# Performance work log

Measured on AMD Instinct MI355X. Metric: run time of the kernel, lower is better.

Reference implementation:

```python
import jax, jax.numpy as jnp
import numpy as np

SCALE = 0.125  # 1/sqrt(embed_dim=64), as passed to Self_Attn in the original


def setup_inputs() -> dict:
    key = jax.random.key(0)
    ks = jax.random.split(key, 6)
    B, S, N, D = 8192, 50, 100000, 64
    nodes = jax.random.randint(ks[0], (B,), 0, N)
    node_seq = jax.random.randint(ks[1], (B, S), 0, N)
    uv2e_weight = jax.random.normal(ks[2], (N, D), dtype=jnp.float32)
    feat_weight = jax.random.normal(ks[3], (N, D), dtype=jnp.float32)
    W1 = jax.random.normal(ks[4], (D, 2 * D), dtype=jnp.float32) * 0.05  # torch Linear weight (out, in)
    b1 = jax.random.normal(ks[5], (D,), dtype=jnp.float32) * 0.05
    return {"nodes": nodes, "node_seq": node_seq, "uv2e_weight": uv2e_weight,
            "feat_weight": feat_weight, "W1": W1, "b1": b1}


def reference(nodes, node_seq, uv2e_weight, feat_weight, W1, b1):
    # gather embeddings: q from self ids, k=v from padded/reversed neighbor sequences
    q = uv2e_weight[nodes]          # [B, D]
    k = uv2e_weight[node_seq]       # [B, S, D]
    v = k                           # same gather in the original
    # Self_Attn: scaled dot-product attention, query length 1 per node
    scores = jnp.einsum('bd,bsd->bs', q, k) * SCALE          # [B, S]
    attn = jax.nn.softmax(scores, axis=-1)                   # [B, S]
    folded = jnp.einsum('bs,bsd->bd', attn, v)                # [B, D]
    # self features (features(nodes).t() in torch yields [B, D])
    self_feats = feat_weight[nodes]                           # [B, D]
    combined = jnp.concatenate([self_feats, folded], axis=1)  # [B, 2D]
    out = jax.nn.relu(combined @ W1.T + b1)                   # [B, D]
    return out
```

## Files before the change

### kernel.cpp

```cpp
#include <hip/hip_runtime.h>
#include <hip/hip_fp16.h>
#include <math.h>


#define DD      64
#define SS      50
#define WPB     8
#define SCALE_L2E 0.180336880f

__device__ __forceinline__ float rdlane_f(float v, int l) {
    return __int_as_float(__builtin_amdgcn_readlane(__float_as_int(v), l));
}

template <int CTRL>
__device__ __forceinline__ float dpp_add(float x) {
    int r = __builtin_amdgcn_update_dpp(0, __float_as_int(x), CTRL, 0xf, 0xf, true);
    return x + __int_as_float(r);
}

__global__ __launch_bounds__(256) void cvt_f32_f16_kernel(
    const float* __restrict__ src, __half* __restrict__ dst, int n8)
{
    int i = blockIdx.x * blockDim.x + threadIdx.x;
    if (i >= n8) return;
    const float4* s4 = (const float4*)src;
    float4 a = s4[2 * i];
    float4 b = s4[2 * i + 1];
    union { __half h[8]; uint4 u; } o;
    o.h[0] = __float2half(a.x); o.h[1] = __float2half(a.y);
    o.h[2] = __float2half(a.z); o.h[3] = __float2half(a.w);
    o.h[4] = __float2half(b.x); o.h[5] = __float2half(b.y);
    o.h[6] = __float2half(b.z); o.h[7] = __float2half(b.w);
    *(uint4*)(dst + 8 * i) = o.u;
}

__global__ __launch_bounds__(512, 6) void folded_encoder_kernel(
    const int*    __restrict__ nodes,
    const int*    __restrict__ node_seq,
    const float*  __restrict__ uv2e,
    const float*  __restrict__ feat,
    const float*  __restrict__ W1,
    const float*  __restrict__ b1,
    const __half* __restrict__ ktab,
    float*        __restrict__ out,
    int B)
{
    __shared__ __align__(16) float Wsw[DD][2 * DD];
    __shared__ int seqbuf[WPB][SS + 2];

    const int tid = threadIdx.x;
    const int wid = tid >> 6;
    const int ln  = tid & 63;
    const int g   = ln >> 4;
    const int t   = ln & 15;

    const int row  = blockIdx.x * WPB + wid;
    const int rowc = row < B ? row : B - 1;

    #pragma unroll
    for (int rep = 0; rep < 16; ++rep) {
        int e = rep * 512 + tid;
        int o = e >> 7;
        int i = e & 127;
        int c = i >> 2, j = i & 3;
        Wsw[o][((c ^ (o & 7)) << 2) + j] = W1[e];
    }
    if (ln < SS) seqbuf[wid][ln] = node_seq[(size_t)rowc * SS + ln];

    const int nid = nodes[rowc];
    const float4 q4 = *(const float4*)(uv2e + (size_t)nid * DD + 4 * t);
    const float4 f4 = *(const float4*)(feat + (size_t)nid * DD + 4 * t);
    const float bias = b1[ln];

    __syncthreads();

    const int start = (25 * g) >> 1;
    const int len   = ((25 * (g + 1)) >> 1) - start;
    const int* sb   = &seqbuf[wid][0];

    int idxr[13];
    #pragma unroll
    for (int s = 0; s < 13; ++s)
        idxr[s] = sb[start + (s < len ? s : 0)];

    uint2 kr[13];
    #pragma unroll
    for (int s = 0; s < 13; ++s)
        kr[s] = *(const uint2*)(ktab + (size_t)idxr[s] * DD + 4 * t);

    float  l   = 0.f;
    float4 acc = make_float4(0.f, 0.f, 0.f, 0.f);
    #pragma unroll
    for (int s = 0; s < 13; ++s) {
        union { uint2 u; __half h[4]; } kw; kw.u = kr[s];
        float k0 = __half2float(kw.h[0]);
        float k1 = __half2float(kw.h[1]);
        float k2 = __half2float(kw.h[2]);
        float k3 = __half2float(kw.h[3]);

        float p = k0 * q4.x + k1 * q4.y + k2 * q4.z + k3 * q4.w;
        p = dpp_add<0xB1>(p);
        p = dpp_add<0x4E>(p);
        p = dpp_add<0x141>(p);
        p = dpp_add<0x140>(p);

        float e  = __builtin_amdgcn_exp2f(p * SCALE_L2E);
        float ee = (s < len) ? e : 0.f;
        l += ee;
        acc.x += ee * k0; acc.y += ee * k1;
        acc.z += ee * k2; acc.w += ee * k3;
    }

    l     += __shfl_xor(l, 16);     l     += __shfl_xor(l, 32);
    acc.x += __shfl_xor(acc.x, 16); acc.x += __shfl_xor(acc.x, 32);
    acc.y += __shfl_xor(acc.y, 16); acc.y += __shfl_xor(acc.y, 32);
    acc.z += __shfl_xor(acc.z, 16); acc.z += __shfl_xor(acc.z, 32);
    acc.w += __shfl_xor(acc.w, 16); acc.w += __shfl_xor(acc.w, 32);

    const float rl = 1.0f / l;
    const float4 fold = make_float4(acc.x * rl, acc.y * rl, acc.z * rl, acc.w * rl);

    float oa0 = bias, oa1 = 0.f;
    const float* wrow = &Wsw[ln][0];
    #pragma unroll
    for (int cc = 0; cc < 32; ++cc) {
        float4 w4 = *(const float4*)&wrow[((cc ^ (ln & 7)) << 2)];
        const int srcl = cc & 15;
        float c0, c1, c2, c3;
        if (cc < 16) {
            c0 = rdlane_f(f4.x, srcl); c1 = rdlane_f(f4.y, srcl);
            c2 = rdlane_f(f4.z, srcl); c3 = rdlane_f(f4.w, srcl);
        } else {
            c0 = rdlane_f(fold.x, srcl); c1 = rdlane_f(fold.y, srcl);
            c2 = rdlane_f(fold.z, srcl); c3 = rdlane_f(fold.w, srcl);
        }
        oa0 += c0 * w4.x + c1 * w4.y;
        oa1 += c2 * w4.z + c3 * w4.w;
    }

    if (row < B)
        out[(size_t)row * DD + ln] = fmaxf(oa0 + oa1, 0.f);
}

extern "C" void kernel_launch(void* const* d_in, const int* in_sizes, int n_in,
                              void* d_out, int out_size, void* d_ws, size_t ws_size,
                              hipStream_t stream) {
    const int*   nodes    = (const int*)  d_in[0];
    const int*   node_seq = (const int*)  d_in[1];
    const float* uv2e     = (const float*)d_in[2];
    const float* feat     = (const float*)d_in[3];
    const float* W1       = (const float*)d_in[4];
    const float* b1       = (const float*)d_in[5];
    float*       out      = (float*)d_out;
    __half*      ktab     = (__half*)d_ws;

    const int B  = in_sizes[0];
    const int NE = in_sizes[2];
    const int n8 = NE / 8;

    cvt_f32_f16_kernel<<<(n8 + 255) / 256, 256, 0, stream>>>(uv2e, ktab, n8);

    const int blocks = (B + WPB - 1) / WPB;
    folded_encoder_kernel<<<blocks, 512, 0, stream>>>(
        nodes, node_seq, uv2e, feat, W1, b1, ktab, out, B);
}
```

Before: 108.3 us.

## Pre-gather query/self features in prep kernel and process two row batches per block

The conversion kernel becomes a combined prep kernel that also gathers the uv2e and feat rows for each node into a contiguous qf buffer. The main kernel now handles two batches of 8 rows per block, which spreads the shared-memory W1 load (now float4-vectorised) across more work. It also reads node_seq indices directly from global memory instead of staging them in shared memory. The block count assumes B is divisible by 16 and the row<B guard no longer protects the q/f loads; the extra qf round-trip adds memory traffic.

```diff
diff --git a/kernel.cpp b/kernel.cpp
--- a/kernel.cpp
+++ b/kernel.cpp
@@ -6,6 +6,7 @@
 #define DD      64
 #define SS      50
 #define WPB     8
+#define BATCHES 2
 #define SCALE_L2E 0.180336880f
 
 __device__ __forceinline__ float rdlane_f(float v, int l) {
@@ -18,35 +19,52 @@
     return x + __int_as_float(r);
 }
 
-__global__ __launch_bounds__(256) void cvt_f32_f16_kernel(
-    const float* __restrict__ src, __half* __restrict__ dst, int n8)
+__global__ __launch_bounds__(256) void prep_kernel(
+    const float* __restrict__ uv2e,
+    const float* __restrict__ feat,
+    const int*   __restrict__ nodes,
+    __half*      __restrict__ ktab,
+    float*       __restrict__ qf,
+    int n8, int nblk_cvt, int B)
 {
-    int i = blockIdx.x * blockDim.x + threadIdx.x;
-    if (i >= n8) return;
-    const float4* s4 = (const float4*)src;
-    float4 a = s4[2 * i];
-    float4 b = s4[2 * i + 1];
-    union { __half h[8]; uint4 u; } o;
-    o.h[0] = __float2half(a.x); o.h[1] = __float2half(a.y);
-    o.h[2] = __float2half(a.z); o.h[3] = __float2half(a.w);
-    o.h[4] = __float2half(b.x); o.h[5] = __float2half(b.y);
-    o.h[6] = __float2half(b.z); o.h[7] = __float2half(b.w);
-    *(uint4*)(dst + 8 * i) = o.u;
+    const int bid = blockIdx.x;
+    const int tid = threadIdx.x;
+    if (bid < nblk_cvt) {
+        int i = bid * 256 + tid;
+        if (i >= n8) return;
+        const float4* s4 = (const float4*)uv2e;
+        float4 a = s4[2 * i];
+        float4 b = s4[2 * i + 1];
+        union { __half h[8]; uint4 u; } o;
+        o.h[0] = __float2half(a.x); o.h[1] = __float2half(a.y);
+        o.h[2] = __float2half(a.z); o.h[3] = __float2half(a.w);
+        o.h[4] = __float2half(b.x); o.h[5] = __float2half(b.y);
+        o.h[6] = __float2half(b.z); o.h[7] = __float2half(b.w);
+        *(uint4*)(ktab + 8 * i) = o.u;
+    } else {
+        int u = (bid - nblk_cvt) * 256 + tid;
+        if (u >= B * 32) return;
+        int row  = u >> 5;
+        int c    = u & 31;
+        int half = c >> 4;
+        int t    = c & 15;
+        int nid  = nodes[row];
+        const float* src = (half ? feat : uv2e) + (size_t)nid * DD + 4 * t;
+        float4 v = *(const float4*)src;
+        *(float4*)(qf + (size_t)row * 128 + half * 64 + 4 * t) = v;
+    }
 }
 
 __global__ __launch_bounds__(512, 6) void folded_encoder_kernel(
-    const int*    __restrict__ nodes,
     const int*    __restrict__ node_seq,
-    const float*  __restrict__ uv2e,
-    const float*  __restrict__ feat,
     const float*  __restrict__ W1,
     const float*  __restrict__ b1,
     const __half* __restrict__ ktab,
+    const float*  __restrict__ qf,
     float*        __restrict__ out,
     int B)
 {
     __shared__ __align__(16) float Wsw[DD][2 * DD];
-    __shared__ int seqbuf[WPB][SS + 2];
 
     const int tid = threadIdx.x;
     const int wid = tid >> 6;
@@ -54,92 +72,98 @@
     const int g   = ln >> 4;
     const int t   = ln & 15;
 
-    const int row  = blockIdx.x * WPB + wid;
-    const int rowc = row < B ? row : B - 1;
-
     #pragma unroll
-    for (int rep = 0; rep < 16; ++rep) {
-        int e = rep * 512 + tid;
-        int o = e >> 7;
-        int i = e & 127;
-        int c = i >> 2, j = i & 3;
-        Wsw[o][((c ^ (o & 7)) << 2) + j] = W1[e];
+    for (int r = 0; r < 4; ++r) {
+        int chunk = r * 512 + tid;
+        int o = chunk >> 5;
+        int c = chunk & 31;
+        float4 w = *(const float4*)(W1 + (size_t)chunk * 4);
+        *(float4*)&Wsw[o][((c ^ (o & 7)) << 2)] = w;
     }
-    if (ln < SS) seqbuf[wid][ln] = node_seq[(size_t)rowc * SS + ln];
-
-    const int nid = nodes[rowc];
-    const float4 q4 = *(const float4*)(uv2e + (size_t)nid * DD + 4 * t);
-    const float4 f4 = *(const float4*)(feat + (size_t)nid * DD + 4 * t);
     const float bias = b1[ln];
-
     __syncthreads();
 
     const int start = (25 * g) >> 1;
     const int len   = ((25 * (g + 1)) >> 1) - start;
-    const int* sb   = &seqbuf[wid][0];
 
-    int idxr[13];
     #pragma unroll
-    for (int s = 0; s < 13; ++s)
-        idxr[s] = sb[start + (s < len ? s : 0)];
+    for (int b = 0; b < BATCHES; ++b) {
+        const int row = (blockIdx.x * BATCHES + b) * WPB + wid;
 
-    uint2 kr[13];
-    #pragma unroll
-    for (int s = 0; s < 13; ++s)
-        kr[s] = *(const uint2*)(ktab + (size_t)idxr[s] * DD + 4 * t);
+        const float4 q4 = *(const float4*)(qf + (size_t)row * 128 + 4 * t);
 
-    float  l   = 0.f;
-    float4 acc = make_float4(0.f, 0.f, 0.f, 0.f);
-    #pragma unroll
-    for (int s = 0; s < 13; ++s) {
-        union { uint2 u; __half h[4]; } kw; kw.u = kr[s];
-        float k0 = __half2float(kw.h[0]);
-        float k1 = __half2float(kw.h[1]);
-        float k2 = __half2float(kw.h[2]);
-        float k3 = __half2float(kw.h[3]);
+        const int* sp = node_seq + (size_t)row * SS + start;
+        int idxa[7], idxb[6];
+        #pragma unroll
+        for (int s = 0; s < 7; ++s) idxa[s] = sp[s < len ? s : 0];
+        #pragma unroll
+        for (int s = 0; s < 6; ++s) idxb[s] = sp[7 + s < len ? 7 + s : 0];
 
-        float p = k0 * q4.x + k1 * q4.y + k2 * q4.z + k3 * q4.w;
-        p = dpp_add<0xB1>(p);
-        p = dpp_add<0x4E>(p);
-        p = dpp_add<0x141>(p);
-        p = dpp_add<0x140>(p);
+        uint2 kra[7], krb[6];
+        #pragma unroll
+        for (int s = 0; s < 7; ++s)
+            kra[s] = *(const uint2*)(ktab + (size_t)idxa[s] * DD + 4 * t);
+        #pragma unroll
+        for (int s = 0; s < 6; ++s)
+            krb[s] = *(const uint2*)(ktab + (size_t)idxb[s] * DD + 4 * t);
 
-        float e  = __builtin_amdgcn_exp2f(p * SCALE_L2E);
-        float ee = (s < len) ? e : 0.f;
-        l += ee;
-        acc.x += ee * k0; acc.y += ee * k1;
-        acc.z += ee * k2; acc.w += ee * k3;
+        float  l   = 0.f;
+        float4 acc = make_float4(0.f, 0.f, 0.f, 0.f);
+
+        #pragma unroll
+        for (int s = 0; s < 13; ++s) {
+            union { uint2 u; __half h[4]; } kw;
+            kw.u = (s < 7) ? kra[s] : krb[s - 7];
+            float k0 = __half2float(kw.h[0]);
+            float k1 = __half2float(kw.h[1]);
+            float k2 = __half2float(kw.h[2]);
+            float k3 = __half2float(kw.h[3]);
+
+            float p = k0 * q4.x + k1 * q4.y + k2 * q4.z + k3 * q4.w;
+            p = dpp_add<0xB1>(p);
+            p = dpp_add<0x4E>(p);
+            p = dpp_add<0x141>(p);
+            p = dpp_add<0x140>(p);
+
+            float e  = __builtin_amdgcn_exp2f(p * SCALE_L2E);
+            float ee = (s < len) ? e : 0.f;
+            l += ee;
+            acc.x += ee * k0; acc.y += ee * k1;
+            acc.z += ee * k2; acc.w += ee * k3;
+        }
+
+        l     += __shfl_xor(l, 16);     l     += __shfl_xor(l, 32);
+        acc.x += __shfl_xor(acc.x, 16); acc.x += __shfl_xor(acc.x, 32);
+        acc.y += __shfl_xor(acc.y, 16); acc.y += __shfl_xor(acc.y, 32);
+        acc.z += __shfl_xor(acc.z, 16); acc.z += __shfl_xor(acc.z, 32);
+        acc.w += __shfl_xor(acc.w, 16); acc.w += __shfl_xor(acc.w, 32);
+
+        const float rl = 1.0f / l;
+        const float4 fold = make_float4(acc.x * rl, acc.y * rl, acc.z * rl, acc.w * rl);
+
+        const float4 f4 = *(const float4*)(qf + (size_t)row * 128 + 64 + 4 * t);
+
+        float oa0 = bias, oa1 = 0.f;
+        const float* wrow = &Wsw[ln][0];
+        #pragma unroll
+        for (int cc = 0; cc < 32; ++cc) {
+            float4 w4 = *(const float4*)&wrow[((cc ^ (ln & 7)) << 2)];
+            const int srcl = cc & 15;
+            float c0, c1, c2, c3;
+            if (cc < 16) {
+                c0 = rdlane_f(f4.x, srcl); c1 = rdlane_f(f4.y, srcl);
+                c2 = rdlane_f(f4.z, srcl); c3 = rdlane_f(f4.w, srcl);
+            } else {
+                c0 = rdlane_f(fold.x, srcl); c1 = rdlane_f(fold.y, srcl);
+                c2 = rdlane_f(fold.z, srcl); c3 = rdlane_f(fold.w, srcl);
+            }
+            oa0 += c0 * w4.x + c1 * w4.y;
+            oa1 += c2 * w4.z + c3 * w4.w;
+        }
+
+        if (row < B)
+            out[(size_t)row * DD + ln] = fmaxf(oa0 + oa1, 0.f);
     }
-
-    l     += __shfl_xor(l, 16);     l     += __shfl_xor(l, 32);
-    acc.x += __shfl_xor(acc.x, 16); acc.x += __shfl_xor(acc.x, 32);
-    acc.y += __shfl_xor(acc.y, 16); acc.y += __shfl_xor(acc.y, 32);
-    acc.z += __shfl_xor(acc.z, 16); acc.z += __shfl_xor(acc.z, 32);
-    acc.w += __shfl_xor(acc.w, 16); acc.w += __shfl_xor(acc.w, 32);
-
-    const float rl = 1.0f / l;
-    const float4 fold = make_float4(acc.x * rl, acc.y * rl, acc.z * rl, acc.w * rl);
-
-    float oa0 = bias, oa1 = 0.f;
-    const float* wrow = &Wsw[ln][0];
-    #pragma unroll
-    for (int cc = 0; cc < 32; ++cc) {
-        float4 w4 = *(const float4*)&wrow[((cc ^ (ln & 7)) << 2)];
-        const int srcl = cc & 15;
-        float c0, c1, c2, c3;
-        if (cc < 16) {
-            c0 = rdlane_f(f4.x, srcl); c1 = rdlane_f(f4.y, srcl);
-            c2 = rdlane_f(f4.z, srcl); c3 = rdlane_f(f4.w, srcl);
-        } else {
-            c0 = rdlane_f(fold.x, srcl); c1 = rdlane_f(fold.y, srcl);
-            c2 = rdlane_f(fold.z, srcl); c3 = rdlane_f(fold.w, srcl);
-        }
-        oa0 += c0 * w4.x + c1 * w4.y;
-        oa1 += c2 * w4.z + c3 * w4.w;
-    }
-
-    if (row < B)
-        out[(size_t)row * DD + ln] = fmaxf(oa0 + oa1, 0.f);
 }
 
 extern "C" void kernel_launch(void* const* d_in, const int* in_sizes, int n_in,
@@ -152,15 +176,20 @@
     const float* W1       = (const float*)d_in[4];
     const float* b1       = (const float*)d_in[5];
     float*       out      = (float*)d_out;
-    __half*      ktab     = (__half*)d_ws;
 
     const int B  = in_sizes[0];
     const int NE = in_sizes[2];
     const int n8 = NE / 8;
 
-    cvt_f32_f16_kernel<<<(n8 + 255) / 256, 256, 0, stream>>>(uv2e, ktab, n8);
+    __half* ktab = (__half*)d_ws;
+    float*  qf   = (float*)((char*)d_ws + (size_t)NE * 2);
 
-    const int blocks = (B + WPB - 1) / WPB;
+    const int nblk_cvt = (n8 + 255) / 256;
+    const int nblk_qf  = (B * 32 + 255) / 256;
+    prep_kernel<<<nblk_cvt + nblk_qf, 256, 0, stream>>>(
+        uv2e, feat, nodes, ktab, qf, n8, nblk_cvt, B);
+
+    const int blocks = B / (BATCHES * WPB);
     folded_encoder_kernel<<<blocks, 512, 0, stream>>>(
-        nodes, node_seq, uv2e, feat, W1, b1, ktab, out, B);
+        node_seq, W1, b1, ktab, qf, out, B);
 }
```

Result: slower. 122.9 us (+13.5%).
